# Kernel tuning notes

Measured on AMD Instinct MI355X. Metric: run time of the kernel, lower is better.

Reference implementation:

```python
import jax, jax.numpy as jnp
import numpy as np

N, K, H, W = 2048, 8, 128, 128
G = 50              # glimpse size (50x50 from tem_rnn input 50*50)
ENC = 100           # glimpse encoder output (relation_rnn input arithmetic)
HID = 256
D_REL = ENC + (3 + 50) * 2 + HID          # 462
D_TEM = G * G + (3 + 50) * 2 + HID        # 2862


def _lin(k, out_d, in_d, scale=0.02):
    k1, k2 = jax.random.split(k)
    return (jax.random.normal(k1, (out_d, in_d), jnp.float32) * scale,
            jax.random.normal(k2, (out_d,), jnp.float32) * scale)


def _lstm_params(k, in_d, hid):
    k1, k2, k3, k4 = jax.random.split(k, 4)
    s = 0.02
    return (jax.random.normal(k1, (4 * hid, in_d), jnp.float32) * s,
            jax.random.normal(k2, (4 * hid, hid), jnp.float32) * s,
            jax.random.normal(k3, (4 * hid,), jnp.float32) * s,
            jax.random.normal(k4, (4 * hid,), jnp.float32) * s)


def lstm_cell(x, h, c, Wih, Whh, bih, bhh):
    g = x @ Wih.T + h @ Whh.T + (bih + bhh)
    i, f, gg, o = jnp.split(g, 4, axis=-1)
    i, f, o = jax.nn.sigmoid(i), jax.nn.sigmoid(f), jax.nn.sigmoid(o)
    c2 = f * c + i * jnp.tanh(gg)
    return o * jnp.tanh(c2), c2


def _bilinear_one(im, py, px):
    # im [H,W]; py,px [G,G] pixel coords; zeros padding like torch grid_sample
    x0 = jnp.floor(px); y0 = jnp.floor(py)
    wx1 = px - x0; wy1 = py - y0
    x0i = x0.astype(jnp.int32); y0i = y0.astype(jnp.int32)

    def gather(yi, xi):
        valid = (yi >= 0) & (yi < H) & (xi >= 0) & (xi < W)
        v = im[jnp.clip(yi, 0, H - 1), jnp.clip(xi, 0, W - 1)]
        return jnp.where(valid, v, 0.0)

    return ((1 - wy1) * (1 - wx1) * gather(y0i, x0i)
            + (1 - wy1) * wx1 * gather(y0i, x0i + 1)
            + wy1 * (1 - wx1) * gather(y0i + 1, x0i)
            + wy1 * wx1 * gather(y0i + 1, x0i + 1))


def stn_glimpse(z_where, img):
    # z_where [n,3] = (scale, tx, ty); theta = [[s,0,tx],[0,s,ty]] (attentive_stn_encode)
    s, tx, ty = z_where[:, 0], z_where[:, 1], z_where[:, 2]
    lin = jnp.linspace(-1.0, 1.0, G)
    gy, gx = jnp.meshgrid(lin, lin, indexing='ij')           # [G,G]
    px = (s[:, None, None] * gx + tx[:, None, None] + 1.0) * 0.5 * (W - 1)
    py = (s[:, None, None] * gy + ty[:, None, None] + 1.0) * 0.5 * (H - 1)
    out = jax.vmap(_bilinear_one)(img, py, px)               # [n,G,G]
    return out.reshape(out.shape[0], G * G)


def setup_inputs() -> dict:
    key = jax.random.key(0)
    ks = jax.random.split(key, 16)
    inp = {
        'img': jax.random.uniform(ks[0], (N, H, W), jnp.float32),
        'z_what_last': jax.random.normal(ks[1], (N, K, 50), jnp.float32),
        'z_where_last': jax.random.normal(ks[2], (N, K, 3), jnp.float32) * 0.3,
        'z_pres_last': jnp.ones((N, K, 1), jnp.float32),
        'hidden_last': jax.random.normal(ks[3], (N, K, HID), jnp.float32),
    }
    inp['W_loca'], inp['b_loca'] = _lin(ks[4], 3, HID)
    inp['Wg'], inp['bg'] = _lin(ks[5], ENC, G * G)
    (inp['Wih_rel'], inp['Whh_rel'], inp['bih_rel'], inp['bhh_rel']) = _lstm_params(ks[6], D_REL, HID)
    (inp['Wih_tem'], inp['Whh_tem'], inp['bih_tem'], inp['bhh_tem']) = _lstm_params(ks[7], D_TEM, HID)
    inp['Wm_wh'], inp['bm_wh'] = _lin(ks[8], 3, HID + 3)
    inp['Ws_wh'], inp['bs_wh'] = _lin(ks[9], 3, HID + 3)
    inp['Wm_wt'], inp['bm_wt'] = _lin(ks[10], 50, 50 + HID + HID)
    inp['Ws_wt'], inp['bs_wt'] = _lin(ks[11], 50, 50 + HID + HID)
    inp['Wm_pr'], inp['bm_pr'] = _lin(ks[12], 1, 50 + 3 + HID + HID)
    inp['Ws_pr'], inp['bs_pr'] = _lin(ks[13], 1, 50 + 3 + HID + HID)
    return inp


def reference(img, z_what_last, z_where_last, z_pres_last, hidden_last,
              W_loca, b_loca, Wg, bg,
              Wih_rel, Whh_rel, bih_rel, bhh_rel,
              Wih_tem, Whh_tem, bih_tem, bhh_tem,
              Wm_wh, bm_wh, Ws_wh, bs_wh,
              Wm_wt, bm_wt, Ws_wt, bs_wt,
              Wm_pr, bm_pr, Ws_pr, bs_pr):
    n = img.shape[0]

    def step(carry, xs):
        h_r, c_r, pzw, pzwhat = carry
        zwl, zwhatl, zpl, hl = xs   # [n,3],[n,50],[n,1],[n,256]
        # prop_loca: relu(linear(hidden)) + z_where_last
        zwb = jax.nn.relu(hl @ W_loca.T + b_loca) + zwl
        # STN glimpse + encode (bias pass)
        enc = jax.nn.relu(stn_glimpse(zwb, img) @ Wg.T + bg)        # [n,100]
        rin = jnp.concatenate([enc, zwl, pzw, zwhatl, pzwhat, hl], -1)  # [n,462]
        h_r2, c_r2 = lstm_cell(rin, h_r, c_r, Wih_rel, Whh_rel, bih_rel, bhh_rel)
        # z_where: latent predictor mean (eval mode)
        zw = jnp.concatenate([zwl, h_r2], -1) @ Wm_wh.T + bm_wh      # [n,3]
        # second STN glimpse with sampled where
        g2 = stn_glimpse(zw, img)                                    # [n,2500]
        tin = jnp.concatenate([g2, zw, pzw, zwhatl, pzwhat, hl], -1) # [n,2862]
        h_t, c_t = lstm_cell(tin, h_r2, c_r2, Wih_tem, Whh_tem, bih_tem, bhh_tem)
        # z_what mean
        zwhat = jnp.concatenate([zwhatl, h_r2, h_t], -1) @ Wm_wt.T + bm_wt  # [n,50]
        # z_pres: deterministic expectation of Bernoulli(mean*std) * previous pres
        zp_cal = jnp.concatenate([zwhat, zw, h_r2, h_t], -1)
        p = jax.nn.sigmoid(zp_cal @ Wm_pr.T + bm_pr) * jax.nn.sigmoid(zp_cal @ Ws_pr.T + bs_pr)
        zp = p * zpl                                                 # [n,1]
        return (h_r2, c_r2, zw, zwhat), (zwhat, zw, zp, h_t)

    carry0 = (jnp.zeros((n, HID), img.dtype), jnp.zeros((n, HID), img.dtype),
              jnp.zeros((n, 3), img.dtype), jnp.zeros((n, 50), img.dtype))
    xs = (jnp.swapaxes(z_where_last, 0, 1), jnp.swapaxes(z_what_last, 0, 1),
          jnp.swapaxes(z_pres_last, 0, 1), jnp.swapaxes(hidden_last, 0, 1))
    _, (zwhat_s, zw_s, zp_s, ht_s) = jax.lax.scan(step, carry0, xs)
    z_what = jnp.swapaxes(zwhat_s, 0, 1)   # [n,K,50]
    z_where = jnp.swapaxes(zw_s, 0, 1)     # [n,K,3]
    z_pres = jnp.swapaxes(zp_s, 0, 1)      # [n,K,1]
    h_temp = jnp.swapaxes(ht_s, 0, 1)      # [n,K,256]
    return z_what, z_where, z_pres, h_temp
```

## Files before the change

### kernel.cpp

```cpp
#include <hip/hip_runtime.h>
#include <hip/hip_bf16.h>
#include <math.h>

typedef __attribute__((ext_vector_type(8))) short bf16x8;
typedef __attribute__((ext_vector_type(4))) float f32x4;
using bf16 = __hip_bfloat16;

constexpr int NN   = 2048;
constexpr int KO   = 8;
constexpr int IH   = 128, IW = 128;
constexpr int GS   = 50;
constexpr int HIDD = 256;
constexpr int RIN_LD = 768;
constexpr int TIN_LD = 3136;
constexpr int G1_LD  = 2560;
constexpr int GROWS  = 64;
constexpr int GROWS2 = 48;

__device__ __forceinline__ float sigm(float x) { return 1.f/(1.f+expf(-x)); }

template<int OUT_BF16, int RELU>
__global__ __launch_bounds__(256, 4) void mfma_gemm(
    const bf16* __restrict__ A, int lda, int Ktot,
    const bf16* __restrict__ Wt, int ldw, int M,
    const float* __restrict__ b1, const float* __restrict__ b2,
    void* __restrict__ Cout, int ldc, int nxb, int Kseg, int sstride)
{
    __shared__ __align__(16) bf16 As[2*4096];
    __shared__ __align__(16) bf16 Bs[2*4096];
    const int b    = blockIdx.x;
    const int xcd  = b & 7;
    const int t    = b >> 3;
    const int n0   = (xcd + 8*(t / nxb))*64;
    const int m0   = (t % nxb)*64;
    const int tid  = threadIdx.x;
    const int w    = tid>>6, lane = tid&63;
    const int wy   = w>>1, wx = w&1;
    const int q    = lane>>4, fr = lane&15;

    const int kbeg = blockIdx.y * Kseg;
    const int kend = min(Ktot, kbeg + Kseg);
    const int nk   = (kend - kbeg) >> 6;

    const int r0   = tid>>3;
    const int csrc = ((tid&7)*8) ^ ((r0&7)<<3);
    const bf16* pa = A + (size_t)(n0 + r0)*lda + kbeg + csrc;
    int wmr0 = m0 + r0;       if (wmr0 > M-1) wmr0 = M-1;
    int wmr1 = m0 + r0 + 32;  if (wmr1 > M-1) wmr1 = M-1;
    const bf16* pb  = Wt + (size_t)wmr0*ldw + kbeg + csrc;
    const bf16* pb1 = Wt + (size_t)wmr1*ldw + kbeg + csrc;

    f32x4 acc[2][2] = {};

    auto stage = [&](int buf, int koff) {
        bf16* la = As + buf*4096 + w*512;
        bf16* lb = Bs + buf*4096 + w*512;
        __builtin_amdgcn_global_load_lds(
            (const __attribute__((address_space(1))) void*)(pa + koff),
            (__attribute__((address_space(3))) void*)la, 16, 0, 0);
        __builtin_amdgcn_global_load_lds(
            (const __attribute__((address_space(1))) void*)(pa + koff + 32*(size_t)lda),
            (__attribute__((address_space(3))) void*)(la + 2048), 16, 0, 0);
        __builtin_amdgcn_global_load_lds(
            (const __attribute__((address_space(1))) void*)(pb + koff),
            (__attribute__((address_space(3))) void*)lb, 16, 0, 0);
        __builtin_amdgcn_global_load_lds(
            (const __attribute__((address_space(1))) void*)(pb1 + koff),
            (__attribute__((address_space(3))) void*)(lb + 2048), 16, 0, 0);
    };

    stage(0, 0);
    __syncthreads();
    int cur = 0;
    for (int kt = 0; kt < nk; ++kt) {
        if (kt + 1 < nk) stage(cur ^ 1, (kt + 1) << 6);
        const bf16* Ab = As + cur*4096;
        const bf16* Bb = Bs + cur*4096;
        bf16x8 av[2][2], bv[2][2];
        #pragma unroll
        for (int i=0;i<2;i++) {
            int r = wy*32 + i*16 + fr;
            int sw = (r&7)<<3, base = r*64;
            av[i][0] = *(const bf16x8*)(Ab + base + ((q*8) ^ sw));
            av[i][1] = *(const bf16x8*)(Ab + base + ((32 + q*8) ^ sw));
        }
        #pragma unroll
        for (int j=0;j<2;j++) {
            int r = wx*32 + j*16 + fr;
            int sw = (r&7)<<3, base = r*64;
            bv[j][0] = *(const bf16x8*)(Bb + base + ((q*8) ^ sw));
            bv[j][1] = *(const bf16x8*)(Bb + base + ((32 + q*8) ^ sw));
        }
        #pragma unroll
        for (int h=0;h<2;h++)
            #pragma unroll
            for (int i=0;i<2;i++)
                #pragma unroll
                for (int j=0;j<2;j++)
                    acc[i][j] = __builtin_amdgcn_mfma_f32_16x16x32_bf16(av[i][h], bv[j][h], acc[i][j], 0, 0, 0);
        __syncthreads();
        cur ^= 1;
    }

    #pragma unroll
    for (int j=0;j<2;j++) {
        int col = m0 + wx*32 + j*16 + fr;
        if (col < M) {
            float bias = 0.f;
            if (blockIdx.y == 0) {
                if (b1) bias += b1[col];
                if (b2) bias += b2[col];
            }
            #pragma unroll
            for (int i=0;i<2;i++) {
                #pragma unroll
                for (int reg=0;reg<4;reg++) {
                    float v = acc[i][j][reg] + bias;
                    if (RELU) v = fmaxf(v, 0.f);
                    size_t idx = (size_t)(n0 + wy*32 + i*16 + q*4 + reg)*ldc + col;
                    if (OUT_BF16) ((bf16*)Cout)[idx] = __float2bfloat16(v);
                    else          ((float*)Cout)[(size_t)blockIdx.y*sstride + idx] = v;
                }
            }
        }
    }
}

__device__ __forceinline__ void glimpse_points_global(const float* __restrict__ im,
                                                      float s, float tx, float ty,
                                                      bf16* __restrict__ drow) {
    const float GXS = 2.0f/49.0f;
    const float txp = tx + 1.0f, typ = ty + 1.0f;
    for (int p2 = threadIdx.x; p2 < 1250; p2 += 256) {
        int i = p2 / 25, j = (p2 - i*25)*2;
        float gy  = fmaf((float)i, GXS, -1.0f);
        float py  = fmaf(s, gy, typ)*63.5f;
        float y0f = floorf(py); float fy = py - y0f; int y0 = (int)y0f;
        float wy0 = ((unsigned)y0     < 128u) ? (1.f - fy) : 0.f;
        float wy1 = ((unsigned)(y0+1) < 128u) ? fy         : 0.f;
        const float* r0 = im + min(max(y0,  0),127)*IW;
        const float* r1 = im + min(max(y0+1,0),127)*IW;
        float gxa = fmaf((float)j, GXS, -1.0f);
        float pxa = fmaf(s, gxa, txp)*63.5f;
        float xa0f = floorf(pxa); float fa = pxa - xa0f; int xa0 = (int)xa0f;
        float wa0 = ((unsigned)xa0     < 128u) ? (1.f - fa) : 0.f;
        float wa1 = ((unsigned)(xa0+1) < 128u) ? fa         : 0.f;
        int xa0c = min(max(xa0,  0),127), xa1c = min(max(xa0+1,0),127);
        float gxb = fmaf((float)(j+1), GXS, -1.0f);
        float pxb = fmaf(s, gxb, txp)*63.5f;
        float xb0f = floorf(pxb); float fb = pxb - xb0f; int xb0 = (int)xb0f;
        float wb0 = ((unsigned)xb0     < 128u) ? (1.f - fb) : 0.f;
        float wb1 = ((unsigned)(xb0+1) < 128u) ? fb         : 0.f;
        int xb0c = min(max(xb0,  0),127), xb1c = min(max(xb0+1,0),127);

        float va = fmaf(wy1, fmaf(wa0, r1[xa0c], wa1*r1[xa1c]),
                   wy0 *     fmaf(wa0, r0[xa0c], wa1*r0[xa1c]));
        float vb = fmaf(wy1, fmaf(wb0, r1[xb0c], wb1*r1[xb1c]),
                   wy0 *     fmaf(wb0, r0[xb0c], wb1*r0[xb1c]));

        bf16 b0 = __float2bfloat16(va), b1 = __float2bfloat16(vb);
        unsigned short u0, u1;
        __builtin_memcpy(&u0, &b0, 2); __builtin_memcpy(&u1, &b1, 2);
        *(unsigned int*)(drow + i*GS + j) = (unsigned)u0 | ((unsigned)u1 << 16);
    }
}

__device__ __forceinline__ void glimpse_points_lds(const float* __restrict__ rows,
                                                   int ylo, int nrows,
                                                   float s, float tx, float ty,
                                                   bf16* __restrict__ drow) {
    const float GXS = 2.0f/49.0f;
    const float txp = tx + 1.0f, typ = ty + 1.0f;
    for (int p2 = threadIdx.x; p2 < 1250; p2 += 256) {
        int i = p2 / 25, j = (p2 - i*25)*2;
        float gy  = fmaf((float)i, GXS, -1.0f);
        float py  = fmaf(s, gy, typ)*63.5f;
        float y0f = floorf(py); float fy = py - y0f; int y0 = (int)y0f;
        float wy0 = ((unsigned)y0     < 128u) ? (1.f - fy) : 0.f;
        float wy1 = ((unsigned)(y0+1) < 128u) ? fy         : 0.f;
        const float* r0 = rows + min(max(y0-ylo,   0), nrows-1)*IW;
        const float* r1 = rows + min(max(y0+1-ylo, 0), nrows-1)*IW;
        float gxa = fmaf((float)j, GXS, -1.0f);
        float pxa = fmaf(s, gxa, txp)*63.5f;
        float xa0f = floorf(pxa); float fa = pxa - xa0f; int xa0 = (int)xa0f;
        float wa0 = ((unsigned)xa0     < 128u) ? (1.f - fa) : 0.f;
        float wa1 = ((unsigned)(xa0+1) < 128u) ? fa         : 0.f;
        int xa0c = min(max(xa0,  0),127), xa1c = min(max(xa0+1,0),127);
        float gxb = fmaf((float)(j+1), GXS, -1.0f);
        float pxb = fmaf(s, gxb, txp)*63.5f;
        float xb0f = floorf(pxb); float fb = pxb - xb0f; int xb0 = (int)xb0f;
        float wb0 = ((unsigned)xb0     < 128u) ? (1.f - fb) : 0.f;
        float wb1 = ((unsigned)(xb0+1) < 128u) ? fb         : 0.f;
        int xb0c = min(max(xb0,  0),127), xb1c = min(max(xb0+1,0),127);
        float va = fmaf(wy1, fmaf(wa0, r1[xa0c], wa1*r1[xa1c]),
                   wy0 *     fmaf(wa0, r0[xa0c], wa1*r0[xa1c]));
        float vb = fmaf(wy1, fmaf(wb0, r1[xb0c], wb1*r1[xb1c]),
                   wy0 *     fmaf(wb0, r0[xb0c], wb1*r0[xb1c]));
        bf16 b0 = __float2bfloat16(va), b1 = __float2bfloat16(vb);
        unsigned short u0, u1;
        __builtin_memcpy(&u0, &b0, 2); __builtin_memcpy(&u1, &b1, 2);
        *(unsigned int*)(drow + i*GS + j) = (unsigned)u0 | ((unsigned)u1 << 16);
    }
}

__global__ __launch_bounds__(256) void glimpse_batch(const float* __restrict__ img,
                                                     const float* __restrict__ z,
                                                     bf16* __restrict__ dst, int ldd,
                                                     bf16* __restrict__ rin,
                                                     const float* __restrict__ z_where_last,
                                                     const float* __restrict__ z_what_last,
                                                     const float* __restrict__ hidden_last,
                                                     int cbase) {
    __shared__ float rows[GROWS*IW];
    int b = blockIdx.x;
    int n = b & (NN-1);
    int sl = b >> 11;
    const float* im = img + (size_t)n*IH*IW;
    float s  = z[b*3+0];
    float tx = z[b*3+1];
    float ty = z[b*3+2];
    bf16* drow = dst + (size_t)b*ldd;

    const float typ = ty + 1.0f;
    float pyA = fmaf(s, -1.f, typ)*63.5f;
    float pyB = fmaf(s,  1.f, typ)*63.5f;
    int ylo = (int)floorf(fminf(pyA, pyB));
    int yhi = (int)floorf(fmaxf(pyA, pyB)) + 1;
    ylo = min(max(ylo, 0), 127);
    yhi = min(max(yhi, 0), 127);
    int nrows = yhi - ylo + 1;

    if (nrows <= GROWS) {
        const float4* src = (const float4*)(im + ylo*IW);
        float4* d4 = (float4*)rows;
        int tot = nrows*(IW/4);
        for (int t = threadIdx.x; t < tot; t += 256) d4[t] = src[t];
        __syncthreads();
        glimpse_points_lds(rows, ylo, nrows, s, tx, ty, drow);
    } else {
        glimpse_points_global(im, s, tx, ty, drow);
    }

    int k = cbase + sl;
    bf16* rrow = rin + (size_t)b*RIN_LD;
    for (int c = threadIdx.x; c < 309; c += 256) {
        float v; int col;
        if (c < 3)       { col = 100 + c;      v = z_where_last[((size_t)n*KO + k)*3 + c]; }
        else if (c < 53) { col = 106 + (c-3);  v = z_what_last[((size_t)n*KO + k)*50 + (c-3)]; }
        else             { col = 206 + (c-53); v = hidden_last[((size_t)n*KO + k)*HIDD + (c-53)]; }
        rrow[col] = __float2bfloat16(v);
    }
}

__global__ __launch_bounds__(256) void rel_glimpse2(
    const float* __restrict__ gates, const float* __restrict__ gates2,
    float* __restrict__ h_r, float* __restrict__ c_r,
    const float* __restrict__ z_where_last,
    const float* __restrict__ Wm_wh, const float* __restrict__ bm_wh,
    float* __restrict__ zw_cur, float* __restrict__ out_zwhere,
    bf16* __restrict__ rin_next, bf16* __restrict__ tin,
    const float* __restrict__ img,
    const float* __restrict__ zw_prev, const float* __restrict__ zwhat_prev,
    const float* __restrict__ z_what_last, const float* __restrict__ hidden_last, int k)
{
    __shared__ float rows[GROWS2*IW];
    __shared__ float hs[256];
    __shared__ float zws[3];
    int n = blockIdx.x, j = threadIdx.x;
    const float* g  = gates  + (size_t)n*1024;
    const float* g2 = gates2 + (size_t)n*1024;
    float ig = sigm(g[j]       + g2[j]);
    float fg = sigm(g[256+j]   + g2[256+j]);
    float gg = tanhf(g[512+j]  + g2[512+j]);
    float og = sigm(g[768+j]   + g2[768+j]);
    int cidx = n*256 + j;
    float c2 = fg*c_r[cidx] + ig*gg;
    float hv = og*tanhf(c2);
    c_r[cidx] = c2;
    h_r[cidx] = hv;
    hs[j] = hv;
    bf16 hb = __float2bfloat16(hv);
    rin_next[(size_t)n*RIN_LD + 462 + j] = hb;
    bf16* trow = tin + (size_t)n*TIN_LD;
    trow[2862 + j] = hb;
    __syncthreads();
    int w = j >> 6, lane = j & 63;
    if (w < 3) {
        const float* wt = Wm_wh + w*259;
        float sa = 0.f;
        for (int i = lane; i < 256; i += 64) sa = fmaf(hs[i], wt[3+i], sa);
        #pragma unroll
        for (int off = 32; off; off >>= 1) sa += __shfl_down(sa, off);
        if (lane == 0) {
            const float* zwl = z_where_last + ((size_t)n*KO + k)*3;
            float acc = bm_wh[w] + sa;
            for (int i = 0; i < 3; i++) acc = fmaf(zwl[i], wt[i], acc);
            zws[w] = acc;
            zw_cur[n*3+w] = acc;
            out_zwhere[((size_t)n*KO + k)*3 + w] = acc;
            bf16 ab = __float2bfloat16(acc);
            rin_next[(size_t)n*RIN_LD + 103 + w] = ab;
            trow[2500 + w] = ab;
        }
    }
    __syncthreads();
    float s = zws[0], tx = zws[1], ty = zws[2];
    const float* im = img + (size_t)n*IH*IW;
    {
        const float typ = ty + 1.0f;
        float pyA = fmaf(s, -1.f, typ)*63.5f;
        float pyB = fmaf(s,  1.f, typ)*63.5f;
        int ylo = (int)floorf(fminf(pyA, pyB));
        int yhi = (int)floorf(fmaxf(pyA, pyB)) + 1;
        ylo = min(max(ylo, 0), 127);
        yhi = min(max(yhi, 0), 127);
        int nrows = yhi - ylo + 1;
        if (nrows <= GROWS2) {
            const float4* src = (const float4*)(im + ylo*IW);
            float4* d4 = (float4*)rows;
            int tot = nrows*(IW/4);
            for (int t = threadIdx.x; t < tot; t += 256) d4[t] = src[t];
            __syncthreads();
            glimpse_points_lds(rows, ylo, nrows, s, tx, ty, trow);
        } else {
            glimpse_points_global(im, s, tx, ty, trow);
        }
    }
    for (int c = 3 + j; c < 362; c += 256) {
        float v;
        if      (c <   6) v = zw_prev[n*3 + c-3];
        else if (c <  56) v = z_what_last[((size_t)n*KO + k)*50 + c-6];
        else if (c < 106) v = zwhat_prev[n*50 + c-56];
        else              v = hidden_last[((size_t)n*KO + k)*HIDD + c-106];
        trow[2500 + c] = __float2bfloat16(v);
    }
}

__global__ void zero_f32(float* __restrict__ p, int n) {
    int i = blockIdx.x*blockDim.x + threadIdx.x;
    if (i < n) p[i] = 0.f;
}

__global__ void repack_w(const float* __restrict__ s1, int K1,
                         const float* __restrict__ s2, int K2,
                         bf16* __restrict__ dst, int ldd, int M) {
    int gid = blockIdx.x*blockDim.x + threadIdx.x;
    if (gid >= M*ldd) return;
    int m = gid / ldd, c = gid - m*ldd;
    float v = 0.f;
    if (c < K1)           v = s1[(size_t)m*K1 + c];
    else if (c < K1+K2)   v = s2[(size_t)m*K2 + (c-K1)];
    dst[gid] = __float2bfloat16(v);
}

__global__ __launch_bounds__(256) void zwb_all_v2(const float* __restrict__ hidden_last,
                                                  const float* __restrict__ z_where_last,
                                                  const float* __restrict__ Wl, const float* __restrict__ bl,
                                                  float* __restrict__ zwb_all) {
    __shared__ float wls[768];
    for (int i = threadIdx.x; i < 768; i += 256) wls[i] = Wl[i];
    __syncthreads();
    int wv = threadIdx.x>>6, lane = threadIdx.x&63;
    int row = blockIdx.x*4 + wv;
    int s = row >> 11, n = row & (NN-1);
    const float* hl = hidden_last + ((size_t)n*KO + s)*HIDD;
    float4 h4 = *(const float4*)(hl + lane*4);
    float s0=0.f, s1=0.f, s2=0.f;
    #pragma unroll
    for (int r4=0;r4<4;r4++) {
        float hv = ((const float*)&h4)[r4];
        int i = lane*4 + r4;
        s0 = fmaf(hv, wls[i],     s0);
        s1 = fmaf(hv, wls[256+i], s1);
        s2 = fmaf(hv, wls[512+i], s2);
    }
    #pragma unroll
    for (int off=32; off; off>>=1) {
        s0 += __shfl_down(s0,off); s1 += __shfl_down(s1,off); s2 += __shfl_down(s2,off);
    }
    if (lane == 0) {
        const float* zwl = z_where_last + ((size_t)n*KO + s)*3;
        zwb_all[row*3+0] = fmaxf(s0+bl[0],0.f) + zwl[0];
        zwb_all[row*3+1] = fmaxf(s1+bl[1],0.f) + zwl[1];
        zwb_all[row*3+2] = fmaxf(s2+bl[2],0.f) + zwl[2];
    }
}

__global__ void zero_rin_carry(bf16* __restrict__ rin0) {
    int gid = blockIdx.x*blockDim.x + threadIdx.x;
    if (gid >= NN*309) return;
    int c = gid % 309, n = gid/309;
    int col = (c < 3) ? 103+c : ((c < 53) ? 156+(c-3) : 462+(c-53));
    rin0[(size_t)n*RIN_LD + col] = __float2bfloat16(0.f);
}

__global__ __launch_bounds__(256) void tem_fused(
    const float* __restrict__ gates, const float* __restrict__ gates2,
    const float* __restrict__ c_r, const float* __restrict__ h_r,
    const float* __restrict__ z_what_last,
    const float* __restrict__ Wm_wt, const float* __restrict__ bm_wt,
    const float* __restrict__ Wm_pr, const float* __restrict__ bm_pr,
    const float* __restrict__ Ws_pr, const float* __restrict__ bs_pr,
    const float* __restrict__ zw_cur, const float* __restrict__ z_pres_last,
    float* __restrict__ zwhat_cur, float* __restrict__ out_zwhat,
    float* __restrict__ out_htemp, float* __restrict__ out_zpres,
    bf16* __restrict__ rin_next, int k)
{
    __shared__ float L[615];
    int n = blockIdx.x, j = threadIdx.x;
    const float* g  = gates  + (size_t)n*1024;
    const float* g2 = gates2 + (size_t)n*1024;
    float ig = sigm(g[j]       + g2[j]);
    float fg = sigm(g[256+j]   + g2[256+j]);
    float gg = tanhf(g[512+j]  + g2[512+j]);
    float og = sigm(g[768+j]   + g2[768+j]);
    float c2 = fg*c_r[n*256+j] + ig*gg;
    float hv = og*tanhf(c2);
    out_htemp[((size_t)n*KO + k)*HIDD + j] = hv;
    L[309+j] = hv;
    L[53+j]  = h_r[n*256+j];
    if (j < 50)      L[j]  = z_what_last[((size_t)n*KO + k)*50 + j];
    else if (j < 53) L[j]  = zw_cur[n*3 + (j-50)];
    __syncthreads();
    if (j < 200) {
        int m = j >> 2, part = j & 3;
        const float* wt = Wm_wt + m*562;
        float s = 0.f;
        for (int i = part; i < 562; i += 4) {
            float v = (i < 50) ? L[i] : L[i+3];
            s = fmaf(v, wt[i], s);
        }
        s += __shfl_down(s, 2);
        s += __shfl_down(s, 1);
        if (part == 0) {
            float acc = s + bm_wt[m];
            zwhat_cur[n*50+m] = acc;
            out_zwhat[((size_t)n*KO + k)*50 + m] = acc;
            rin_next[(size_t)n*RIN_LD + 156 + m] = __float2bfloat16(acc);
            L[565+m] = acc;
        }
    }
    __syncthreads();
    if (j < 64) {
        float s1 = 0.f, s2 = 0.f;
        for (int i = j; i < 565; i += 64) {
            float v = (i < 50) ? L[565+i] : L[i];
            s1 = fmaf(v, Wm_pr[i], s1);
            s2 = fmaf(v, Ws_pr[i], s2);
        }
        #pragma unroll
        for (int off = 32; off; off >>= 1) { s1 += __shfl_down(s1,off); s2 += __shfl_down(s2,off); }
        if (j == 0) {
            float p = sigm(s1 + bm_pr[0]) * sigm(s2 + bs_pr[0]);
            out_zpres[(size_t)n*KO + k] = p * z_pres_last[(size_t)n*KO + k];
        }
    }
}

extern "C" void kernel_launch(void* const* d_in, const int* in_sizes, int n_in,
                              void* d_out, int out_size, void* d_ws, size_t ws_size,
                              hipStream_t stream) {
    (void)in_sizes; (void)n_in; (void)out_size;
    const float* img          = (const float*)d_in[0];
    const float* z_what_last  = (const float*)d_in[1];
    const float* z_where_last = (const float*)d_in[2];
    const float* z_pres_last  = (const float*)d_in[3];
    const float* hidden_last  = (const float*)d_in[4];
    const float* W_loca = (const float*)d_in[5];
    const float* b_loca = (const float*)d_in[6];
    const float* Wg     = (const float*)d_in[7];
    const float* bg     = (const float*)d_in[8];
    const float* Wih_rel = (const float*)d_in[9];
    const float* Whh_rel = (const float*)d_in[10];
    const float* bih_rel = (const float*)d_in[11];
    const float* bhh_rel = (const float*)d_in[12];
    const float* Wih_tem = (const float*)d_in[13];
    const float* Whh_tem = (const float*)d_in[14];
    const float* bih_tem = (const float*)d_in[15];
    const float* bhh_tem = (const float*)d_in[16];
    const float* Wm_wh = (const float*)d_in[17];
    const float* bm_wh = (const float*)d_in[18];
    const float* Wm_wt = (const float*)d_in[21];
    const float* bm_wt = (const float*)d_in[22];
    const float* Wm_pr = (const float*)d_in[25];
    const float* bm_pr = (const float*)d_in[26];
    const float* Ws_pr = (const float*)d_in[27];
    const float* bs_pr = (const float*)d_in[28];

    char* base_p = (char*)d_ws;
    size_t off = 0;
    auto carve = [&](size_t bytes) -> char* {
        char* r = base_p + off;
        off += (bytes + 255) & ~(size_t)255;
        return r;
    };
    bf16*  tin      = (bf16*) carve((size_t)NN*TIN_LD*2);
    float* gates    = (float*)carve((size_t)2*NN*1024*4);
    bf16*  W_tem    = (bf16*) carve((size_t)1024*TIN_LD*2);
    bf16*  W_rel    = (bf16*) carve((size_t)1024*RIN_LD*2);
    bf16*  Wg_bf    = (bf16*) carve((size_t)100*G1_LD*2);
    float* zwb_all  = (float*)carve((size_t)KO*NN*3*4);
    float* h_r      = (float*)carve((size_t)NN*HIDD*4);
    float* c_r      = (float*)carve((size_t)NN*HIDD*4);
    float* zw1      = (float*)carve((size_t)NN*3*4);
    float* zwhat1   = (float*)carve((size_t)NN*50*4);
    float* zw0      = (float*)carve((size_t)NN*3*4);
    float* zwhat0   = (float*)carve((size_t)NN*50*4);
    size_t fixed_bytes = off;
    float* gates2 = gates + (size_t)NN*1024;

    int CH = 1;
    for (int cand : {8, 4, 2}) {
        size_t need = fixed_bytes
                    + (((size_t)cand*NN*G1_LD*2 + 255) & ~(size_t)255)
                    + (((size_t)cand*NN*RIN_LD*2 + 255) & ~(size_t)255);
        if (need <= ws_size) { CH = cand; break; }
    }
    bf16* g1 = nullptr; int g1ld;
    bf16* rin;
    if (CH > 1) {
        g1   = (bf16*)carve((size_t)CH*NN*G1_LD*2);
        rin  = (bf16*)carve((size_t)CH*NN*RIN_LD*2);
        g1ld = G1_LD;
    } else {
        rin  = (bf16*)carve((size_t)NN*RIN_LD*2);
        g1   = tin;
        g1ld = TIN_LD;
    }

    float* out        = (float*)d_out;
    float* out_zwhat  = out;
    float* out_zwhere = out + (size_t)NN*KO*50;
    float* out_zpres  = out_zwhere + (size_t)NN*KO*3;
    float* out_htemp  = out_zpres + (size_t)NN*KO;

    {
        int nz = NN*(HIDD + 3 + 50);
        zero_f32<<<(nz+255)/256, 256, 0, stream>>>(c_r, nz);
    }
    zero_rin_carry<<<(NN*309+255)/256, 256, 0, stream>>>(rin);
    repack_w<<<((1024*RIN_LD)+255)/256, 256, 0, stream>>>(Wih_rel, 462, Whh_rel, 256, W_rel, RIN_LD, 1024);
    repack_w<<<((1024*TIN_LD)+255)/256, 256, 0, stream>>>(Wih_tem, 2862, Whh_tem, 256, W_tem, TIN_LD, 1024);
    repack_w<<<((100*G1_LD)+255)/256, 256, 0, stream>>>(Wg, 2500, nullptr, 0, Wg_bf, G1_LD, 100);
    zwb_all_v2<<<KO*NN/4, 256, 0, stream>>>(hidden_last, z_where_last, W_loca, b_loca, zwb_all);

    const int GSTR = NN*1024;
    const int KSEG_REL = 384;
    const int KSEG_TEM = 1600;

    for (int cbase = 0; cbase < KO; cbase += CH) {
        glimpse_batch<<<CH*NN, 256, 0, stream>>>(img, zwb_all + (size_t)cbase*NN*3, g1, g1ld,
                                                 rin, z_where_last, z_what_last, hidden_last, cbase);
        mfma_gemm<1,1><<<dim3(2*CH*32,1), 256, 0, stream>>>(g1, g1ld, G1_LD, Wg_bf, G1_LD, 100,
                                                            bg, nullptr, rin, RIN_LD, 2, G1_LD, 0);

        for (int s = 0; s < CH; ++s) {
            int k = cbase + s;
            bf16* rin_k  = rin + (size_t)s*NN*RIN_LD;
            bf16* rin_nx = rin + (size_t)((s+1)%CH)*NN*RIN_LD;
            float* zw_cur     = (k & 1) ? zw1 : zw0;
            float* zw_prev    = (k & 1) ? zw0 : zw1;
            float* zwhat_cur  = (k & 1) ? zwhat1 : zwhat0;
            float* zwhat_prev = (k & 1) ? zwhat0 : zwhat1;

            mfma_gemm<0,0><<<dim3(512,2), 256, 0, stream>>>(rin_k, RIN_LD, RIN_LD, W_rel, RIN_LD, 1024,
                                                            bih_rel, bhh_rel, gates, 1024, 16, KSEG_REL, GSTR);
            rel_glimpse2<<<NN, 256, 0, stream>>>(gates, gates2, h_r, c_r, z_where_last, Wm_wh, bm_wh,
                                                 zw_cur, out_zwhere, rin_nx, tin,
                                                 img, zw_prev, zwhat_prev, z_what_last, hidden_last, k);
            mfma_gemm<0,0><<<dim3(512,2), 256, 0, stream>>>(tin, TIN_LD, TIN_LD, W_tem, TIN_LD, 1024,
                                                            bih_tem, bhh_tem, gates, 1024, 16, KSEG_TEM, GSTR);
            tem_fused<<<NN, 256, 0, stream>>>(gates, gates2, c_r, h_r, z_what_last, Wm_wt, bm_wt, Wm_pr, bm_pr, Ws_pr, bs_pr,
                                              zw_cur, z_pres_last, zwhat_cur, out_zwhat, out_htemp, out_zpres, rin_nx, k);
        }
    }
}
```

Before: 1.198 ms.

## Stage whole image in LDS once per sample for all glimpse slots; transpose z_what weights

The glimpse kernel now launches one 512-thread block per sample, loads the full 128x128 image into shared memory once, and samples every glimpse slot of the chunk from it. The old design issued one block per (slot, sample) and re-read the needed rows each time. In rel_glimpse2 the row-staging LDS path is removed and sampling reads global memory directly. The z_what projection in tem_fused uses a pre-transposed, padded weight matrix so that adjacent threads read adjacent addresses, with the partial sums reduced through shared memory. The 64KB LDS buffer limits occupancy to few blocks per CU, and direct global gathers in rel_glimpse2 may cost more than the old staged reads.

```diff
diff --git a/kernel.cpp b/kernel.cpp
--- a/kernel.cpp
+++ b/kernel.cpp
@@ -14,8 +14,6 @@
 constexpr int RIN_LD = 768;
 constexpr int TIN_LD = 3136;
 constexpr int G1_LD  = 2560;
-constexpr int GROWS  = 64;
-constexpr int GROWS2 = 48;
 
 __device__ __forceinline__ float sigm(float x) { return 1.f/(1.f+expf(-x)); }
 
@@ -165,85 +163,72 @@
     }
 }
 
-__device__ __forceinline__ void glimpse_points_lds(const float* __restrict__ rows,
-                                                   int ylo, int nrows,
-                                                   float s, float tx, float ty,
-                                                   bf16* __restrict__ drow) {
+__device__ __forceinline__ void sample_pair_lds(const float* __restrict__ im_s,
+                                                float s, float txp, float typ,
+                                                int i, int j, bf16* __restrict__ drow) {
     const float GXS = 2.0f/49.0f;
-    const float txp = tx + 1.0f, typ = ty + 1.0f;
-    for (int p2 = threadIdx.x; p2 < 1250; p2 += 256) {
+    float gy  = fmaf((float)i, GXS, -1.0f);
+    float py  = fmaf(s, gy, typ)*63.5f;
+    float y0f = floorf(py); float fy = py - y0f; int y0 = (int)y0f;
+    float wy0 = ((unsigned)y0     < 128u) ? (1.f - fy) : 0.f;
+    float wy1 = ((unsigned)(y0+1) < 128u) ? fy         : 0.f;
+    const float* r0 = im_s + min(max(y0,  0),127)*IW;
+    const float* r1 = im_s + min(max(y0+1,0),127)*IW;
+    float gxa = fmaf((float)j, GXS, -1.0f);
+    float pxa = fmaf(s, gxa, txp)*63.5f;
+    float xa0f = floorf(pxa); float fa = pxa - xa0f; int xa0 = (int)xa0f;
+    float wa0 = ((unsigned)xa0     < 128u) ? (1.f - fa) : 0.f;
+    float wa1 = ((unsigned)(xa0+1) < 128u) ? fa         : 0.f;
+    int xa0c = min(max(xa0,  0),127), xa1c = min(max(xa0+1,0),127);
+    float gxb = fmaf((float)(j+1), GXS, -1.0f);
+    float pxb = fmaf(s, gxb, txp)*63.5f;
+    float xb0f = floorf(pxb); float fb = pxb - xb0f; int xb0 = (int)xb0f;
+    float wb0 = ((unsigned)xb0     < 128u) ? (1.f - fb) : 0.f;
+    float wb1 = ((unsigned)(xb0+1) < 128u) ? fb         : 0.f;
+    int xb0c = min(max(xb0,  0),127), xb1c = min(max(xb0+1,0),127);
+    float va = fmaf(wy1, fmaf(wa0, r1[xa0c], wa1*r1[xa1c]),
+               wy0 *     fmaf(wa0, r0[xa0c], wa1*r0[xa1c]));
+    float vb = fmaf(wy1, fmaf(wb0, r1[xb0c], wb1*r1[xb1c]),
+               wy0 *     fmaf(wb0, r0[xb0c], wb1*r0[xb1c]));
+    bf16 b0 = __float2bfloat16(va), b1 = __float2bfloat16(vb);
+    unsigned short u0, u1;
+    __builtin_memcpy(&u0, &b0, 2); __builtin_memcpy(&u1, &b1, 2);
+    *(unsigned int*)(drow + i*GS + j) = (unsigned)u0 | ((unsigned)u1 << 16);
+}
+
+__global__ __launch_bounds__(512) void glimpse_all(const float* __restrict__ img,
+                                                   const float* __restrict__ zwb,
+                                                   bf16* __restrict__ dst, int ldd,
+                                                   bf16* __restrict__ rin,
+                                                   const float* __restrict__ z_where_last,
+                                                   const float* __restrict__ z_what_last,
+                                                   const float* __restrict__ hidden_last,
+                                                   int cbase, int CH) {
+    __shared__ float im_s[IH*IW];
+    const int n = blockIdx.x;
+    const float* im = img + (size_t)n*IH*IW;
+    {
+        const float4* s4 = (const float4*)im;
+        float4* d4 = (float4*)im_s;
+        #pragma unroll
+        for (int t = threadIdx.x; t < IH*IW/4; t += 512) d4[t] = s4[t];
+    }
+    __syncthreads();
+
+    const int tot = CH*1250;
+    for (int p = threadIdx.x; p < tot; p += 512) {
+        int sl = p / 1250, p2 = p - sl*1250;
         int i = p2 / 25, j = (p2 - i*25)*2;
-        float gy  = fmaf((float)i, GXS, -1.0f);
-        float py  = fmaf(s, gy, typ)*63.5f;
-        float y0f = floorf(py); float fy = py - y0f; int y0 = (int)y0f;
-        float wy0 = ((unsigned)y0     < 128u) ? (1.f - fy) : 0.f;
-        float wy1 = ((unsigned)(y0+1) < 128u) ? fy         : 0.f;
-        const float* r0 = rows + min(max(y0-ylo,   0), nrows-1)*IW;
-        const float* r1 = rows + min(max(y0+1-ylo, 0), nrows-1)*IW;
-        float gxa = fmaf((float)j, GXS, -1.0f);
-        float pxa = fmaf(s, gxa, txp)*63.5f;
-        float xa0f = floorf(pxa); float fa = pxa - xa0f; int xa0 = (int)xa0f;
-        float wa0 = ((unsigned)xa0     < 128u) ? (1.f - fa) : 0.f;
-        float wa1 = ((unsigned)(xa0+1) < 128u) ? fa         : 0.f;
-        int xa0c = min(max(xa0,  0),127), xa1c = min(max(xa0+1,0),127);
-        float gxb = fmaf((float)(j+1), GXS, -1.0f);
-        float pxb = fmaf(s, gxb, txp)*63.5f;
-        float xb0f = floorf(pxb); float fb = pxb - xb0f; int xb0 = (int)xb0f;
-        float wb0 = ((unsigned)xb0     < 128u) ? (1.f - fb) : 0.f;
-        float wb1 = ((unsigned)(xb0+1) < 128u) ? fb         : 0.f;
-        int xb0c = min(max(xb0,  0),127), xb1c = min(max(xb0+1,0),127);
-        float va = fmaf(wy1, fmaf(wa0, r1[xa0c], wa1*r1[xa1c]),
-                   wy0 *     fmaf(wa0, r0[xa0c], wa1*r0[xa1c]));
-        float vb = fmaf(wy1, fmaf(wb0, r1[xb0c], wb1*r1[xb1c]),
-                   wy0 *     fmaf(wb0, r0[xb0c], wb1*r0[xb1c]));
-        bf16 b0 = __float2bfloat16(va), b1 = __float2bfloat16(vb);
-        unsigned short u0, u1;
-        __builtin_memcpy(&u0, &b0, 2); __builtin_memcpy(&u1, &b1, 2);
-        *(unsigned int*)(drow + i*GS + j) = (unsigned)u0 | ((unsigned)u1 << 16);
-    }
-}
-
-__global__ __launch_bounds__(256) void glimpse_batch(const float* __restrict__ img,
-                                                     const float* __restrict__ z,
-                                                     bf16* __restrict__ dst, int ldd,
-                                                     bf16* __restrict__ rin,
-                                                     const float* __restrict__ z_where_last,
-                                                     const float* __restrict__ z_what_last,
-                                                     const float* __restrict__ hidden_last,
-                                                     int cbase) {
-    __shared__ float rows[GROWS*IW];
-    int b = blockIdx.x;
-    int n = b & (NN-1);
-    int sl = b >> 11;
-    const float* im = img + (size_t)n*IH*IW;
-    float s  = z[b*3+0];
-    float tx = z[b*3+1];
-    float ty = z[b*3+2];
-    bf16* drow = dst + (size_t)b*ldd;
-
-    const float typ = ty + 1.0f;
-    float pyA = fmaf(s, -1.f, typ)*63.5f;
-    float pyB = fmaf(s,  1.f, typ)*63.5f;
-    int ylo = (int)floorf(fminf(pyA, pyB));
-    int yhi = (int)floorf(fmaxf(pyA, pyB)) + 1;
-    ylo = min(max(ylo, 0), 127);
-    yhi = min(max(yhi, 0), 127);
-    int nrows = yhi - ylo + 1;
-
-    if (nrows <= GROWS) {
-        const float4* src = (const float4*)(im + ylo*IW);
-        float4* d4 = (float4*)rows;
-        int tot = nrows*(IW/4);
-        for (int t = threadIdx.x; t < tot; t += 256) d4[t] = src[t];
-        __syncthreads();
-        glimpse_points_lds(rows, ylo, nrows, s, tx, ty, drow);
-    } else {
-        glimpse_points_global(im, s, tx, ty, drow);
-    }
-
-    int k = cbase + sl;
-    bf16* rrow = rin + (size_t)b*RIN_LD;
-    for (int c = threadIdx.x; c < 309; c += 256) {
+        const float* zr = zwb + (size_t)(sl*NN + n)*3;
+        float s = zr[0], txp = zr[1] + 1.0f, typ = zr[2] + 1.0f;
+        sample_pair_lds(im_s, s, txp, typ, i, j, dst + (size_t)(sl*NN + n)*ldd);
+    }
+
+    const int tot2 = CH*309;
+    for (int t = threadIdx.x; t < tot2; t += 512) {
+        int sl = t / 309, c = t - sl*309;
+        int k = cbase + sl;
+        bf16* rrow = rin + (size_t)(sl*NN + n)*RIN_LD;
         float v; int col;
         if (c < 3)       { col = 100 + c;      v = z_where_last[((size_t)n*KO + k)*3 + c]; }
         else if (c < 53) { col = 106 + (c-3);  v = z_what_last[((size_t)n*KO + k)*50 + (c-3)]; }
@@ -263,7 +248,6 @@
     const float* __restrict__ zw_prev, const float* __restrict__ zwhat_prev,
     const float* __restrict__ z_what_last, const float* __restrict__ hidden_last, int k)
 {
-    __shared__ float rows[GROWS2*IW];
     __shared__ float hs[256];
     __shared__ float zws[3];
     int n = blockIdx.x, j = threadIdx.x;
@@ -305,27 +289,7 @@
     }
     __syncthreads();
     float s = zws[0], tx = zws[1], ty = zws[2];
-    const float* im = img + (size_t)n*IH*IW;
-    {
-        const float typ = ty + 1.0f;
-        float pyA = fmaf(s, -1.f, typ)*63.5f;
-        float pyB = fmaf(s,  1.f, typ)*63.5f;
-        int ylo = (int)floorf(fminf(pyA, pyB));
-        int yhi = (int)floorf(fmaxf(pyA, pyB)) + 1;
-        ylo = min(max(ylo, 0), 127);
-        yhi = min(max(yhi, 0), 127);
-        int nrows = yhi - ylo + 1;
-        if (nrows <= GROWS2) {
-            const float4* src = (const float4*)(im + ylo*IW);
-            float4* d4 = (float4*)rows;
-            int tot = nrows*(IW/4);
-            for (int t = threadIdx.x; t < tot; t += 256) d4[t] = src[t];
-            __syncthreads();
-            glimpse_points_lds(rows, ylo, nrows, s, tx, ty, trow);
-        } else {
-            glimpse_points_global(im, s, tx, ty, trow);
-        }
-    }
+    glimpse_points_global(img + (size_t)n*IH*IW, s, tx, ty, trow);
     for (int c = 3 + j; c < 362; c += 256) {
         float v;
         if      (c <   6) v = zw_prev[n*3 + c-3];
@@ -351,6 +315,13 @@
     if (c < K1)           v = s1[(size_t)m*K1 + c];
     else if (c < K1+K2)   v = s2[(size_t)m*K2 + (c-K1)];
     dst[gid] = __float2bfloat16(v);
+}
+
+__global__ void transpose_wmwt(const float* __restrict__ W, float* __restrict__ Wt) {
+    int gid = blockIdx.x*blockDim.x + threadIdx.x;
+    if (gid >= 576*64) return;
+    int i = gid >> 6, m = gid & 63;
+    Wt[gid] = (m < 50 && i < 562) ? W[(size_t)m*562 + i] : 0.f;
 }
 
 __global__ __launch_bounds__(256) void zwb_all_v2(const float* __restrict__ hidden_last,
@@ -398,7 +369,7 @@
     const float* __restrict__ gates, const float* __restrict__ gates2,
     const float* __restrict__ c_r, const float* __restrict__ h_r,
     const float* __restrict__ z_what_last,
-    const float* __restrict__ Wm_wt, const float* __restrict__ bm_wt,
+    const float* __restrict__ wt_t, const float* __restrict__ bm_wt,
     const float* __restrict__ Wm_pr, const float* __restrict__ bm_pr,
     const float* __restrict__ Ws_pr, const float* __restrict__ bs_pr,
     const float* __restrict__ zw_cur, const float* __restrict__ z_pres_last,
@@ -407,6 +378,7 @@
     bf16* __restrict__ rin_next, int k)
 {
     __shared__ float L[615];
+    __shared__ float part[4][64];
     int n = blockIdx.x, j = threadIdx.x;
     const float* g  = gates  + (size_t)n*1024;
     const float* g2 = gates2 + (size_t)n*1024;
@@ -422,23 +394,22 @@
     if (j < 50)      L[j]  = z_what_last[((size_t)n*KO + k)*50 + j];
     else if (j < 53) L[j]  = zw_cur[n*3 + (j-50)];
     __syncthreads();
-    if (j < 200) {
-        int m = j >> 2, part = j & 3;
-        const float* wt = Wm_wt + m*562;
-        float s = 0.f;
-        for (int i = part; i < 562; i += 4) {
+    {
+        int m = j & 63, grp = j >> 6;
+        float sa = 0.f;
+        for (int i = grp; i < 562; i += 4) {
             float v = (i < 50) ? L[i] : L[i+3];
-            s = fmaf(v, wt[i], s);
-        }
-        s += __shfl_down(s, 2);
-        s += __shfl_down(s, 1);
-        if (part == 0) {
-            float acc = s + bm_wt[m];
-            zwhat_cur[n*50+m] = acc;
-            out_zwhat[((size_t)n*KO + k)*50 + m] = acc;
-            rin_next[(size_t)n*RIN_LD + 156 + m] = __float2bfloat16(acc);
-            L[565+m] = acc;
-        }
+            sa = fmaf(v, wt_t[i*64 + m], sa);
+        }
+        part[grp][m] = sa;
+    }
+    __syncthreads();
+    if (j < 50) {
+        float acc = part[0][j] + part[1][j] + part[2][j] + part[3][j] + bm_wt[j];
+        zwhat_cur[n*50+j] = acc;
+        out_zwhat[((size_t)n*KO + k)*50 + j] = acc;
+        rin_next[(size_t)n*RIN_LD + 156 + j] = __float2bfloat16(acc);
+        L[565+j] = acc;
     }
     __syncthreads();
     if (j < 64) {
@@ -499,6 +470,7 @@
     bf16*  W_tem    = (bf16*) carve((size_t)1024*TIN_LD*2);
     bf16*  W_rel    = (bf16*) carve((size_t)1024*RIN_LD*2);
     bf16*  Wg_bf    = (bf16*) carve((size_t)100*G1_LD*2);
+    float* wt_t     = (float*)carve((size_t)576*64*4);
     float* zwb_all  = (float*)carve((size_t)KO*NN*3*4);
     float* h_r      = (float*)carve((size_t)NN*HIDD*4);
     float* c_r      = (float*)carve((size_t)NN*HIDD*4);
@@ -542,6 +514,7 @@
     repack_w<<<((1024*RIN_LD)+255)/256, 256, 0, stream>>>(Wih_rel, 462, Whh_rel, 256, W_rel, RIN_LD, 1024);
     repack_w<<<((1024*TIN_LD)+255)/256, 256, 0, stream>>>(Wih_tem, 2862, Whh_tem, 256, W_tem, TIN_LD, 1024);
     repack_w<<<((100*G1_LD)+255)/256, 256, 0, stream>>>(Wg, 2500, nullptr, 0, Wg_bf, G1_LD, 100);
+    transpose_wmwt<<<(576*64+255)/256, 256, 0, stream>>>(Wm_wt, wt_t);
     zwb_all_v2<<<KO*NN/4, 256, 0, stream>>>(hidden_last, z_where_last, W_loca, b_loca, zwb_all);
 
     const int GSTR = NN*1024;
@@ -549,8 +522,8 @@
     const int KSEG_TEM = 1600;
 
     for (int cbase = 0; cbase < KO; cbase += CH) {
-        glimpse_batch<<<CH*NN, 256, 0, stream>>>(img, zwb_all + (size_t)cbase*NN*3, g1, g1ld,
-                                                 rin, z_where_last, z_what_last, hidden_last, cbase);
+        glimpse_all<<<NN, 512, 0, stream>>>(img, zwb_all + (size_t)cbase*NN*3, g1, g1ld,
+                                            rin, z_where_last, z_what_last, hidden_last, cbase, CH);
         mfma_gemm<1,1><<<dim3(2*CH*32,1), 256, 0, stream>>>(g1, g1ld, G1_LD, Wg_bf, G1_LD, 100,
                                                             bg, nullptr, rin, RIN_LD, 2, G1_LD, 0);
 
@@ -570,7 +543,7 @@
                                                  img, zw_prev, zwhat_prev, z_what_last, hidden_last, k);
             mfma_gemm<0,0><<<dim3(512,2), 256, 0, stream>>>(tin, TIN_LD, TIN_LD, W_tem, TIN_LD, 1024,
                                                             bih_tem, bhh_tem, gates, 1024, 16, KSEG_TEM, GSTR);
-            tem_fused<<<NN, 256, 0, stream>>>(gates, gates2, c_r, h_r, z_what_last, Wm_wt, bm_wt, Wm_pr, bm_pr, Ws_pr, bs_pr,
+            tem_fused<<<NN, 256, 0, stream>>>(gates, gates2, c_r, h_r, z_what_last, wt_t, bm_wt, Wm_pr, bm_pr, Ws_pr, bs_pr,
                                               zw_cur, z_pres_last, zwhat_cur, out_zwhat, out_htemp, out_zpres, rin_nx, k);
         }
     }
```

New measurement: 1.138 ms. 1.05x faster.
